# Kernel optimization log

Hardware: AMD Instinct MI355X
Metric: run time of the kernel (lower is better)

Reference implementation:

```python
import jax, jax.numpy as jnp
import numpy as np

B, S, D, H = 2, 2048, 1024, 16
DH = D // H  # 64


def setup_inputs() -> dict:
    key = jax.random.key(0)
    ks = jax.random.split(key, 9)
    def rn(k, shape, scale=1.0):
        return jax.random.normal(k, shape, dtype=jnp.float32) * scale
    w_scale = 1.0 / np.sqrt(D)
    return {
        "queries": rn(ks[0], (B, S, D)),
        "keys": rn(ks[1], (B, S, D)),
        "values": rn(ks[2], (B, S, D)),
        "Wq": rn(ks[3], (D, D), w_scale),
        "bq": rn(ks[4], (D,), w_scale),
        "Wk": rn(ks[5], (D, D), w_scale),
        "bk": rn(ks[6], (D,), w_scale),
        "Wv": rn(ks[7], (D, D), w_scale),
        "bv": rn(ks[8], (D,), w_scale),
    }


def _split_heads(x):
    # torch: cat(split(x, DH, dim=-1), dim=0) -> index (h*B + b); equivalent to
    # [B,S,H,DH] -> [H,B,S,DH]
    bsz, slen, _ = x.shape
    return x.reshape(bsz, slen, H, DH).transpose(2, 0, 1, 3)


def reference(queries, keys, values, Wq, bq, Wk, bk, Wv, bv):
    # Linear projections (W stored so that y = x @ W + b)
    Q = queries @ Wq + bq
    K = keys @ Wk + bk
    V = values @ Wv + bv

    Qh = _split_heads(Q)  # [H,B,S,DH]
    Kh = _split_heads(K)
    Vh = _split_heads(V)

    scale = 1.0 / jnp.sqrt(jnp.asarray(DH, dtype=Qh.dtype))
    scores = jnp.einsum("hbqd,hbkd->hbqk", Qh, Kh) * scale  # [H,B,S,S]
    attn = jax.nn.softmax(scores, axis=-1)  # dropout_rate=0 -> identity
    out = jnp.einsum("hbqk,hbkd->hbqd", attn, Vh)  # [H,B,S,DH]

    # torch: cat(split(out, B, dim=0), dim=2) -> [B,S,H*DH] with head h in slice h
    out = out.transpose(1, 2, 0, 3).reshape(queries.shape[0], queries.shape[1], D)
    return out + queries  # residual; NOTE: W_O is defined but unused in the original forward
```

## Files before the change

### kernel.cpp

```cpp
#include <hip/hip_runtime.h>
#include <hip/hip_bf16.h>
#include <math.h>

#define BB 2
#define SS 2048
#define DD 1024
#define HH 16
#define DHH 64
#define MM (BB * SS)

typedef float f32x4 __attribute__((ext_vector_type(4)));
typedef float f32x16 __attribute__((ext_vector_type(16)));
typedef __bf16 bf16x8 __attribute__((ext_vector_type(8)));
typedef unsigned int u32x2 __attribute__((ext_vector_type(2)));

#define N_QKV ((size_t)MM * DD)
#define N_W   ((size_t)DD * DD)

__device__ unsigned short g_X [3][N_QKV];
__device__ unsigned short g_Q [N_QKV];
__device__ unsigned short g_K [N_QKV];
__device__ unsigned short g_Vt[N_QKV];
__device__ unsigned short g_Wt[3][N_W];

__device__ __forceinline__ unsigned short f2bu(float f) {
    unsigned u = __float_as_uint(f);
    unsigned r = u + 0x7FFFu + ((u >> 16) & 1u);
    return (unsigned short)(r >> 16);
}

union FragU { uint4 u; bf16x8 v; unsigned short s[8]; };
static __device__ __forceinline__ bf16x8 ldfrag(const unsigned short* p) {
    FragU f; f.u = *(const uint4*)p; return f.v;
}

static __device__ __forceinline__ unsigned pkbf(float a, float b) {
    union { __bf16 h[2]; unsigned u; } w;
    w.h[0] = (__bf16)a; w.h[1] = (__bf16)b;
    return w.u;
}

static __device__ __forceinline__ float fexp2(float x) {
#if __has_builtin(__builtin_amdgcn_exp2f)
    return __builtin_amdgcn_exp2f(x);
#else
    float r;
    asm("v_exp_f32 %0, %1" : "=v"(r) : "v"(x));
    return r;
#endif
}

static __device__ __forceinline__ void plswap(unsigned &a, unsigned &b) {
#if __has_builtin(__builtin_amdgcn_permlane32_swap)
    u32x2 r = __builtin_amdgcn_permlane32_swap((int)a, (int)b, false, false);
    a = r[0]; b = r[1];
#else
    asm volatile("v_permlane32_swap_b32 %0, %1" : "+v"(a), "+v"(b));
#endif
}

__global__ __launch_bounds__(256) void cvt3(
        const float* __restrict__ x0, const float* __restrict__ x1,
        const float* __restrict__ x2, unsigned short* __restrict__ X)
{
    const float* src = blockIdx.y == 0 ? x0 : (blockIdx.y == 1 ? x1 : x2);
    unsigned short* dst = X + (size_t)blockIdx.y * N_QKV;
    const size_t i = ((size_t)blockIdx.x * 256 + threadIdx.x) * 4;
    const float4 v = *(const float4*)(src + i);
    ushort4 s;
    s.x = f2bu(v.x); s.y = f2bu(v.y); s.z = f2bu(v.z); s.w = f2bu(v.w);
    *(ushort4*)(dst + i) = s;
}

__global__ __launch_bounds__(256) void transpose_w3(
        const float* __restrict__ W0, const float* __restrict__ W1,
        const float* __restrict__ W2, unsigned short* __restrict__ Wt3)
{
    const float* W = blockIdx.z == 0 ? W0 : (blockIdx.z == 1 ? W1 : W2);
    unsigned short* Wt = Wt3 + (size_t)blockIdx.z * N_W;
    __shared__ float Ts[64][65];
    const int t = threadIdx.x;
    const int k0 = blockIdx.y * 64, n0 = blockIdx.x * 64;
#pragma unroll
    for (int i = 0; i < 16; ++i) {
        const int f = t + 256 * i, r = f >> 6, c = f & 63;
        Ts[r][c] = W[(size_t)(k0 + r) * DD + n0 + c];
    }
    __syncthreads();
#pragma unroll
    for (int i = 0; i < 16; ++i) {
        const int f = t + 256 * i, r = f >> 6, c = f & 63;
        Wt[(size_t)(n0 + r) * DD + k0 + c] = f2bu(Ts[c][r]);
    }
}

__global__ __launch_bounds__(256) void proj3(
        const unsigned short* __restrict__ X, const unsigned short* __restrict__ Wt3,
        const float* __restrict__ bq, const float* __restrict__ bk,
        const float* __restrict__ bv,
        unsigned short* __restrict__ Qp, unsigned short* __restrict__ Kp,
        unsigned short* __restrict__ Vtp)
{
    const int z = blockIdx.z;
    const unsigned short* xb = X   + (size_t)z * N_QKV;
    const unsigned short* Wt = Wt3 + (size_t)z * N_W;
    const float* bias = z == 0 ? bq : (z == 1 ? bk : bv);
    const float scale = z == 0 ? 0.18033688011112042f : 1.0f;

    __shared__ unsigned short As[128][72];
    __shared__ unsigned short Bs[128][72];
    const int t = threadIdx.x, lane = t & 63, w = t >> 6;
    const int q = lane >> 4, li = lane & 15;
    const int wm = (w >> 1) * 64, wn = (w & 1) * 64;
    const int m0 = blockIdx.y * 128, n0 = blockIdx.x * 128;
    const int rs = t >> 3, cs = (t & 7) * 8;

    f32x4 acc[4][4];
#pragma unroll
    for (int mt = 0; mt < 4; ++mt)
#pragma unroll
        for (int nt = 0; nt < 4; ++nt) acc[mt][nt] = (f32x4)0.f;

    uint4 pa0, pa1, pa2, pa3, pb0, pb1, pb2, pb3;
#define PROJ_LD(kk) \
    pa0 = *(const uint4*)(xb + (size_t)(m0 + rs      ) * DD + (kk) + cs); \
    pa1 = *(const uint4*)(xb + (size_t)(m0 + rs + 32 ) * DD + (kk) + cs); \
    pa2 = *(const uint4*)(xb + (size_t)(m0 + rs + 64 ) * DD + (kk) + cs); \
    pa3 = *(const uint4*)(xb + (size_t)(m0 + rs + 96 ) * DD + (kk) + cs); \
    pb0 = *(const uint4*)(Wt + (size_t)(n0 + rs      ) * DD + (kk) + cs); \
    pb1 = *(const uint4*)(Wt + (size_t)(n0 + rs + 32 ) * DD + (kk) + cs); \
    pb2 = *(const uint4*)(Wt + (size_t)(n0 + rs + 64 ) * DD + (kk) + cs); \
    pb3 = *(const uint4*)(Wt + (size_t)(n0 + rs + 96 ) * DD + (kk) + cs);

    PROJ_LD(0)

    for (int kk = 0; kk < DD; kk += 64) {
        *(uint4*)&As[rs     ][cs] = pa0;
        *(uint4*)&As[rs + 32][cs] = pa1;
        *(uint4*)&As[rs + 64][cs] = pa2;
        *(uint4*)&As[rs + 96][cs] = pa3;
        *(uint4*)&Bs[rs     ][cs] = pb0;
        *(uint4*)&Bs[rs + 32][cs] = pb1;
        *(uint4*)&Bs[rs + 64][cs] = pb2;
        *(uint4*)&Bs[rs + 96][cs] = pb3;
        __syncthreads();
        if (kk + 64 < DD) { PROJ_LD(kk + 64) }
#pragma unroll
        for (int ks = 0; ks < 64; ks += 32) {
            bf16x8 a[4], b[4];
#pragma unroll
            for (int mt = 0; mt < 4; ++mt) a[mt] = ldfrag(&As[wm + mt * 16 + li][ks + q * 8]);
#pragma unroll
            for (int nt = 0; nt < 4; ++nt) b[nt] = ldfrag(&Bs[wn + nt * 16 + li][ks + q * 8]);
#pragma unroll
            for (int mt = 0; mt < 4; ++mt)
#pragma unroll
                for (int nt = 0; nt < 4; ++nt)
                    acc[mt][nt] = __builtin_amdgcn_mfma_f32_16x16x32_bf16(
                        a[mt], b[nt], acc[mt][nt], 0, 0, 0);
        }
        __syncthreads();
    }
#undef PROJ_LD

    float bvv[4];
#pragma unroll
    for (int nt = 0; nt < 4; ++nt) bvv[nt] = bias[n0 + wn + nt * 16 + li];

    if (z < 2) {
        unsigned short* out = z == 0 ? Qp : Kp;
#pragma unroll
        for (int mt = 0; mt < 4; ++mt)
#pragma unroll
            for (int nt = 0; nt < 4; ++nt)
#pragma unroll
                for (int reg = 0; reg < 4; ++reg) {
                    const int m = m0 + wm + mt * 16 + q * 4 + reg;
                    out[(size_t)m * DD + n0 + wn + nt * 16 + li] =
                        f2bu((acc[mt][nt][reg] + bvv[nt]) * scale);
                }
    } else {
        const int b = m0 >> 11;
        const int h = (n0 + wn) >> 6;
#pragma unroll
        for (int mt = 0; mt < 4; ++mt)
#pragma unroll
            for (int nt = 0; nt < 4; ++nt) {
                const int s = (m0 & (SS - 1)) + wm + mt * 16 + q * 4;
                const int dh = nt * 16 + li;
                ushort4 sv;
                sv.x = f2bu(acc[mt][nt][0] + bvv[nt]);
                sv.y = f2bu(acc[mt][nt][1] + bvv[nt]);
                sv.z = f2bu(acc[mt][nt][2] + bvv[nt]);
                sv.w = f2bu(acc[mt][nt][3] + bvv[nt]);
                *(ushort4*)(Vtp + ((size_t)((b * HH + h) * DHH + dh)) * SS + s) = sv;
            }
    }
}

__global__ __launch_bounds__(512, 2) void attn8(
        const unsigned short* __restrict__ Qg, const unsigned short* __restrict__ Kg,
        const unsigned short* __restrict__ Vtg,
        const float* __restrict__ queries, float* __restrict__ outp)
{
    __shared__ unsigned short KVb[2][2][2][64][64];
    __shared__ float Lp[2][4][32];

    const int t = threadIdx.x, lane = t & 63;
    const int g  = t >> 8;
    const int wg = (t >> 6) & 3;
    const int col = lane & 31;
    const int hi  = lane >> 5;
    const int qt = blockIdx.x, h = blockIdx.y, b = blockIdx.z;

    const int tg = t & 255;
    const int sr = tg >> 3;
    const int sc = tg & 7;

    unsigned short (*Kb)[64][64] = KVb[g][0];
    unsigned short (*Vb)[64][64] = KVb[g][1];

    const unsigned short* Kbase = Kg  + (size_t)(b * SS) * DD + h * DHH;
    const unsigned short* Vbase = Vtg + ((size_t)((b * HH + h) * DHH)) * SS;

    bf16x8 qa[4];
    {
        const unsigned short* qp =
            Qg + (size_t)(b * SS + qt * 128 + wg * 32 + col) * DD + h * DHH + hi * 8;
#pragma unroll
        for (int i = 0; i < 4; ++i) qa[i] = ldfrag(qp + i * 16);
    }

    f32x16 o0 = (f32x16)0.f, o1 = (f32x16)0.f;
    float lsum = 0.f;
    const int xr2 = (col ^ (col >> 3)) & 7;
    const int wsw = (sr ^ (sr >> 3)) & 7;
    const int kvofs = g << 10;

    uint4 k0, k1, v0, v1;
#define LD_TILE(s0) \
    k0 = *(const uint4*)(Kbase + (size_t)((s0) + sr     ) * DD + sc * 8); \
    k1 = *(const uint4*)(Kbase + (size_t)((s0) + sr + 32) * DD + sc * 8); \
    v0 = *(const uint4*)(Vbase + (size_t)(sr     ) * SS + (s0) + sc * 8); \
    v1 = *(const uint4*)(Vbase + (size_t)(sr + 32) * SS + (s0) + sc * 8);

#define ST_TILE(buf) \
    *(uint4*)&Kb[buf][sr     ][(sc ^ wsw) * 8]     = k0; \
    *(uint4*)&Kb[buf][sr + 32][(sc ^ wsw ^ 4) * 8] = k1; \
    *(uint4*)&Vb[buf][sr     ][(sc ^ wsw) * 8]     = v0; \
    *(uint4*)&Vb[buf][sr + 32][(sc ^ wsw ^ 4) * 8] = v1;

    LD_TILE(kvofs)
    ST_TILE(0)
    __syncthreads();

    const int NT = 16;
#pragma unroll 2
    for (int kt = 0; kt < NT; ++kt) {
        const int cur = kt & 1;
        if (kt + 1 < NT) { LD_TILE(kvofs + (kt + 1) * 64) }

        f32x16 st0 = (f32x16)0.f, st1 = (f32x16)0.f;
#pragma unroll
        for (int i = 0; i < 4; ++i) {
            const int sl = (i * 2 + hi) ^ xr2;
            bf16x8 ka0 = ldfrag(&Kb[cur][col     ][sl * 8]);
            bf16x8 ka1 = ldfrag(&Kb[cur][col + 32][(sl ^ 4) * 8]);
            st0 = __builtin_amdgcn_mfma_f32_32x32x16_bf16(ka0, qa[i], st0, 0, 0, 0);
            st1 = __builtin_amdgcn_mfma_f32_32x32x16_bf16(ka1, qa[i], st1, 0, 0, 0);
        }

        unsigned pkw[4][4];
        float ls = 0.f;
#pragma unroll
        for (int s = 0; s < 2; ++s) {
            float pe[8];
#pragma unroll
            for (int r = 0; r < 8; ++r) pe[r] = fexp2(st0[8 * s + r]);
            ls += ((pe[0] + pe[1]) + (pe[2] + pe[3])) + ((pe[4] + pe[5]) + (pe[6] + pe[7]));
            pkw[s][0] = pkbf(pe[0], pe[1]); pkw[s][1] = pkbf(pe[2], pe[3]);
            pkw[s][2] = pkbf(pe[4], pe[5]); pkw[s][3] = pkbf(pe[6], pe[7]);
        }
#pragma unroll
        for (int s = 0; s < 2; ++s) {
            float pe[8];
#pragma unroll
            for (int r = 0; r < 8; ++r) pe[r] = fexp2(st1[8 * s + r]);
            ls += ((pe[0] + pe[1]) + (pe[2] + pe[3])) + ((pe[4] + pe[5]) + (pe[6] + pe[7]));
            pkw[2 + s][0] = pkbf(pe[0], pe[1]); pkw[2 + s][1] = pkbf(pe[2], pe[3]);
            pkw[2 + s][2] = pkbf(pe[4], pe[5]); pkw[2 + s][3] = pkbf(pe[6], pe[7]);
        }
        lsum += ls;

        if (kt + 1 < NT) { ST_TILE(cur ^ 1) }

#pragma unroll
        for (int c = 0; c < 4; ++c) {
            unsigned a0 = pkw[c][0], b0 = pkw[c][2];
            unsigned a1 = pkw[c][1], b1 = pkw[c][3];
            plswap(a0, b0);
            plswap(a1, b1);
            FragU pf;
            pf.u.x = a0; pf.u.y = a1; pf.u.z = b0; pf.u.w = b1;

            const int vl = (c * 2 + hi) ^ xr2;
            bf16x8 vb0 = ldfrag(&Vb[cur][col     ][vl * 8]);
            bf16x8 vb1 = ldfrag(&Vb[cur][col + 32][(vl ^ 4) * 8]);
            o0 = __builtin_amdgcn_mfma_f32_32x32x16_bf16(pf.v, vb0, o0, 0, 0, 0);
            o1 = __builtin_amdgcn_mfma_f32_32x32x16_bf16(pf.v, vb1, o1, 0, 0, 0);
        }
        __syncthreads();
    }
#undef LD_TILE
#undef ST_TILE

    const float lt = lsum + __shfl_xor(lsum, 32);
    float* Ob = (float*)KVb;
    const int obase = wg * 64 + lane;
    if (g == 1) {
#pragma unroll
        for (int r = 0; r < 16; ++r) {
            Ob[r * 256 + obase]        = o0[r];
            Ob[(16 + r) * 256 + obase] = o1[r];
        }
    }
    if (lane < 32) Lp[g][wg][lane] = lt;
    __syncthreads();

    if (g == 0) {
        const size_t gbase = (size_t)(b * SS + qt * 128 + wg * 32) * DD + h * DHH + col;
#pragma unroll
        for (int reg = 0; reg < 16; ++reg) {
            const int rl = (reg & 3) + 8 * (reg >> 2) + 4 * hi;
            const float li = 1.f / (Lp[0][wg][rl] + Lp[1][wg][rl]);
            const size_t gaddr = gbase + (size_t)rl * DD;
            outp[gaddr]      = (o0[reg] + Ob[reg * 256 + obase]) * li + queries[gaddr];
            outp[gaddr + 32] = (o1[reg] + Ob[(16 + reg) * 256 + obase]) * li + queries[gaddr + 32];
        }
    }
}

extern "C" void kernel_launch(void* const* d_in, const int* in_sizes, int n_in,
                              void* d_out, int out_size, void* d_ws, size_t ws_size,
                              hipStream_t stream) {
    const float* queries = (const float*)d_in[0];
    const float* keys    = (const float*)d_in[1];
    const float* values  = (const float*)d_in[2];
    const float* Wq      = (const float*)d_in[3];
    const float* bq      = (const float*)d_in[4];
    const float* Wk      = (const float*)d_in[5];
    const float* bk      = (const float*)d_in[6];
    const float* Wv      = (const float*)d_in[7];
    const float* bv      = (const float*)d_in[8];
    float* outp = (float*)d_out;

    const size_t need = (6 * N_QKV + 3 * N_W) * sizeof(unsigned short);
    unsigned short *Xp, *Qp, *Kp, *Vtp, *Wtp;
    if (ws_size >= need) {
        Xp  = (unsigned short*)d_ws;
        Qp  = Xp + 3 * N_QKV;
        Kp  = Qp + N_QKV;
        Vtp = Kp + N_QKV;
        Wtp = Vtp + N_QKV;
    } else {
        hipGetSymbolAddress((void**)&Xp,  HIP_SYMBOL(g_X));
        hipGetSymbolAddress((void**)&Qp,  HIP_SYMBOL(g_Q));
        hipGetSymbolAddress((void**)&Kp,  HIP_SYMBOL(g_K));
        hipGetSymbolAddress((void**)&Vtp, HIP_SYMBOL(g_Vt));
        hipGetSymbolAddress((void**)&Wtp, HIP_SYMBOL(g_Wt));
    }

    const dim3 bp(256);
    cvt3<<<dim3(MM * DD / 1024, 3), bp, 0, stream>>>(queries, keys, values, Xp);
    transpose_w3<<<dim3(16, 16, 3), bp, 0, stream>>>(Wq, Wk, Wv, Wtp);
    proj3<<<dim3(8, 32, 3), bp, 0, stream>>>(Xp, Wtp, bq, bk, bv, Qp, Kp, Vtp);
    attn8<<<dim3(SS / 128, HH, BB), dim3(512), 0, stream>>>(Qp, Kp, Vtp, queries, outp);
}
```

Before: 202.7 us.

## Deepen KV prefetch to two tiles, add MFMA priority, remap block order

The attention kernel now keeps two register sets of K/V tiles in flight, loading tile kt+2 while computing tile kt, so global load latency is hidden over a longer window. MFMA sections are wrapped in s_setprio to favour matrix issue over other waves. The grid is flattened to 1D and blocks are remapped so the eight consecutive block IDs cover different head/batch pairs, which changes L2 locality across XCDs. The extra prefetch registers raise register pressure under the 512x2 launch bound and may cause spills.

```diff
diff --git a/kernel.cpp b/kernel.cpp
--- a/kernel.cpp
+++ b/kernel.cpp
@@ -198,7 +198,7 @@
     }
 }
 
-__global__ __launch_bounds__(512, 2) void attn8(
+__global__ __launch_bounds__(512, 2) void attn9(
         const unsigned short* __restrict__ Qg, const unsigned short* __restrict__ Kg,
         const unsigned short* __restrict__ Vtg,
         const float* __restrict__ queries, float* __restrict__ outp)
@@ -211,7 +211,13 @@
     const int wg = (t >> 6) & 3;
     const int col = lane & 31;
     const int hi  = lane >> 5;
-    const int qt = blockIdx.x, h = blockIdx.y, b = blockIdx.z;
+
+    const int bid = blockIdx.x;
+    const int slot = bid >> 3;
+    const int p = (bid & 7) + 8 * (slot >> 4);
+    const int qt = slot & 15;
+    const int h = p & 15;
+    const int b = p >> 4;
 
     const int tg = t & 255;
     const int sr = tg >> 3;
@@ -237,82 +243,95 @@
     const int wsw = (sr ^ (sr >> 3)) & 7;
     const int kvofs = g << 10;
 
-    uint4 k0, k1, v0, v1;
-#define LD_TILE(s0) \
-    k0 = *(const uint4*)(Kbase + (size_t)((s0) + sr     ) * DD + sc * 8); \
-    k1 = *(const uint4*)(Kbase + (size_t)((s0) + sr + 32) * DD + sc * 8); \
-    v0 = *(const uint4*)(Vbase + (size_t)(sr     ) * SS + (s0) + sc * 8); \
-    v1 = *(const uint4*)(Vbase + (size_t)(sr + 32) * SS + (s0) + sc * 8);
-
-#define ST_TILE(buf) \
-    *(uint4*)&Kb[buf][sr     ][(sc ^ wsw) * 8]     = k0; \
-    *(uint4*)&Kb[buf][sr + 32][(sc ^ wsw ^ 4) * 8] = k1; \
-    *(uint4*)&Vb[buf][sr     ][(sc ^ wsw) * 8]     = v0; \
-    *(uint4*)&Vb[buf][sr + 32][(sc ^ wsw ^ 4) * 8] = v1;
-
-    LD_TILE(kvofs)
-    ST_TILE(0)
+    uint4 aK0, aK1, aV0, aV1, bK0, bK1, bV0, bV1;
+#define LD_SET(K0, K1, V0, V1, s0) \
+    K0 = *(const uint4*)(Kbase + (size_t)((s0) + sr     ) * DD + sc * 8); \
+    K1 = *(const uint4*)(Kbase + (size_t)((s0) + sr + 32) * DD + sc * 8); \
+    V0 = *(const uint4*)(Vbase + (size_t)(sr     ) * SS + (s0) + sc * 8); \
+    V1 = *(const uint4*)(Vbase + (size_t)(sr + 32) * SS + (s0) + sc * 8);
+
+#define ST_SET(K0, K1, V0, V1, buf) \
+    *(uint4*)&Kb[buf][sr     ][(sc ^ wsw) * 8]     = K0; \
+    *(uint4*)&Kb[buf][sr + 32][(sc ^ wsw ^ 4) * 8] = K1; \
+    *(uint4*)&Vb[buf][sr     ][(sc ^ wsw) * 8]     = V0; \
+    *(uint4*)&Vb[buf][sr + 32][(sc ^ wsw ^ 4) * 8] = V1;
+
+#define KT_BODY(CUR, LDG, STG, LDQ4, STQ4)                                    \
+    {                                                                         \
+        if (LDG) { LD_SET LDQ4 }                                              \
+                       \
+        f32x16 st0 = (f32x16)0.f, st1 = (f32x16)0.f;                          \
+        __builtin_amdgcn_s_setprio(1);                                        \
+        _Pragma("unroll")                                                     \
+        for (int i = 0; i < 4; ++i) {                                         \
+            const int sl = (i * 2 + hi) ^ xr2;                                \
+            bf16x8 ka0 = ldfrag(&Kb[CUR][col     ][sl * 8]);                  \
+            bf16x8 ka1 = ldfrag(&Kb[CUR][col + 32][(sl ^ 4) * 8]);            \
+            st0 = __builtin_amdgcn_mfma_f32_32x32x16_bf16(ka0, qa[i], st0, 0, 0, 0); \
+            st1 = __builtin_amdgcn_mfma_f32_32x32x16_bf16(ka1, qa[i], st1, 0, 0, 0); \
+        }                                                                     \
+        __builtin_amdgcn_s_setprio(0);                                        \
+                                 \
+        unsigned pkw[4][4];                                                   \
+        float ls = 0.f;                                                       \
+        _Pragma("unroll")                                                     \
+        for (int s = 0; s < 2; ++s) {                                         \
+            float pe[8];                                                      \
+            _Pragma("unroll")                                                 \
+            for (int r = 0; r < 8; ++r) pe[r] = fexp2(st0[8 * s + r]);        \
+            ls += ((pe[0] + pe[1]) + (pe[2] + pe[3])) + ((pe[4] + pe[5]) + (pe[6] + pe[7])); \
+            pkw[s][0] = pkbf(pe[0], pe[1]); pkw[s][1] = pkbf(pe[2], pe[3]);   \
+            pkw[s][2] = pkbf(pe[4], pe[5]); pkw[s][3] = pkbf(pe[6], pe[7]);   \
+        }                                                                     \
+        _Pragma("unroll")                                                     \
+        for (int s = 0; s < 2; ++s) {                                         \
+            float pe[8];                                                      \
+            _Pragma("unroll")                                                 \
+            for (int r = 0; r < 8; ++r) pe[r] = fexp2(st1[8 * s + r]);        \
+            ls += ((pe[0] + pe[1]) + (pe[2] + pe[3])) + ((pe[4] + pe[5]) + (pe[6] + pe[7])); \
+            pkw[2 + s][0] = pkbf(pe[0], pe[1]); pkw[2 + s][1] = pkbf(pe[2], pe[3]); \
+            pkw[2 + s][2] = pkbf(pe[4], pe[5]); pkw[2 + s][3] = pkbf(pe[6], pe[7]); \
+        }                                                                     \
+        lsum += ls;                                                           \
+             \
+        if (STG) { ST_SET STQ4 }                                              \
+          \
+        __builtin_amdgcn_s_setprio(1);                                        \
+        _Pragma("unroll")                                                     \
+        for (int c = 0; c < 4; ++c) {                                         \
+            unsigned A0 = pkw[c][0], B0 = pkw[c][2];                          \
+            unsigned A1 = pkw[c][1], B1 = pkw[c][3];                          \
+            plswap(A0, B0);                                                   \
+            plswap(A1, B1);                                                   \
+            FragU pf;                                                         \
+            pf.u.x = A0; pf.u.y = A1; pf.u.z = B0; pf.u.w = B1;               \
+            const int vl = (c * 2 + hi) ^ xr2;                                \
+            bf16x8 vb0 = ldfrag(&Vb[CUR][col     ][vl * 8]);                  \
+            bf16x8 vb1 = ldfrag(&Vb[CUR][col + 32][(vl ^ 4) * 8]);            \
+            o0 = __builtin_amdgcn_mfma_f32_32x32x16_bf16(pf.v, vb0, o0, 0, 0, 0); \
+            o1 = __builtin_amdgcn_mfma_f32_32x32x16_bf16(pf.v, vb1, o1, 0, 0, 0); \
+        }                                                                     \
+        __builtin_amdgcn_s_setprio(0);                                        \
+        __syncthreads();                                                      \
+    }
+
+    const int NT = 16;
+    LD_SET(aK0, aK1, aV0, aV1, kvofs)
+    LD_SET(bK0, bK1, bV0, bV1, kvofs + 64)
+    ST_SET(aK0, aK1, aV0, aV1, 0)
     __syncthreads();
 
-    const int NT = 16;
-#pragma unroll 2
-    for (int kt = 0; kt < NT; ++kt) {
-        const int cur = kt & 1;
-        if (kt + 1 < NT) { LD_TILE(kvofs + (kt + 1) * 64) }
-
-        f32x16 st0 = (f32x16)0.f, st1 = (f32x16)0.f;
-#pragma unroll
-        for (int i = 0; i < 4; ++i) {
-            const int sl = (i * 2 + hi) ^ xr2;
-            bf16x8 ka0 = ldfrag(&Kb[cur][col     ][sl * 8]);
-            bf16x8 ka1 = ldfrag(&Kb[cur][col + 32][(sl ^ 4) * 8]);
-            st0 = __builtin_amdgcn_mfma_f32_32x32x16_bf16(ka0, qa[i], st0, 0, 0, 0);
-            st1 = __builtin_amdgcn_mfma_f32_32x32x16_bf16(ka1, qa[i], st1, 0, 0, 0);
-        }
-
-        unsigned pkw[4][4];
-        float ls = 0.f;
-#pragma unroll
-        for (int s = 0; s < 2; ++s) {
-            float pe[8];
-#pragma unroll
-            for (int r = 0; r < 8; ++r) pe[r] = fexp2(st0[8 * s + r]);
-            ls += ((pe[0] + pe[1]) + (pe[2] + pe[3])) + ((pe[4] + pe[5]) + (pe[6] + pe[7]));
-            pkw[s][0] = pkbf(pe[0], pe[1]); pkw[s][1] = pkbf(pe[2], pe[3]);
-            pkw[s][2] = pkbf(pe[4], pe[5]); pkw[s][3] = pkbf(pe[6], pe[7]);
-        }
-#pragma unroll
-        for (int s = 0; s < 2; ++s) {
-            float pe[8];
-#pragma unroll
-            for (int r = 0; r < 8; ++r) pe[r] = fexp2(st1[8 * s + r]);
-            ls += ((pe[0] + pe[1]) + (pe[2] + pe[3])) + ((pe[4] + pe[5]) + (pe[6] + pe[7]));
-            pkw[2 + s][0] = pkbf(pe[0], pe[1]); pkw[2 + s][1] = pkbf(pe[2], pe[3]);
-            pkw[2 + s][2] = pkbf(pe[4], pe[5]); pkw[2 + s][3] = pkbf(pe[6], pe[7]);
-        }
-        lsum += ls;
-
-        if (kt + 1 < NT) { ST_TILE(cur ^ 1) }
-
-#pragma unroll
-        for (int c = 0; c < 4; ++c) {
-            unsigned a0 = pkw[c][0], b0 = pkw[c][2];
-            unsigned a1 = pkw[c][1], b1 = pkw[c][3];
-            plswap(a0, b0);
-            plswap(a1, b1);
-            FragU pf;
-            pf.u.x = a0; pf.u.y = a1; pf.u.z = b0; pf.u.w = b1;
-
-            const int vl = (c * 2 + hi) ^ xr2;
-            bf16x8 vb0 = ldfrag(&Vb[cur][col     ][vl * 8]);
-            bf16x8 vb1 = ldfrag(&Vb[cur][col + 32][(vl ^ 4) * 8]);
-            o0 = __builtin_amdgcn_mfma_f32_32x32x16_bf16(pf.v, vb0, o0, 0, 0, 0);
-            o1 = __builtin_amdgcn_mfma_f32_32x32x16_bf16(pf.v, vb1, o1, 0, 0, 0);
-        }
-        __syncthreads();
-    }
-#undef LD_TILE
-#undef ST_TILE
+    for (int kt = 0; kt < NT; kt += 2) {
+        KT_BODY(0, (kt + 2 < NT), (kt + 1 < NT),
+                (aK0, aK1, aV0, aV1, kvofs + (kt + 2) * 64),
+                (bK0, bK1, bV0, bV1, 1))
+        KT_BODY(1, (kt + 3 < NT), (kt + 2 < NT),
+                (bK0, bK1, bV0, bV1, kvofs + (kt + 3) * 64),
+                (aK0, aK1, aV0, aV1, 0))
+    }
+#undef KT_BODY
+#undef LD_SET
+#undef ST_SET
 
     const float lt = lsum + __shfl_xor(lsum, 32);
     float* Ob = (float*)KVb;
@@ -374,5 +393,5 @@
     cvt3<<<dim3(MM * DD / 1024, 3), bp, 0, stream>>>(queries, keys, values, Xp);
     transpose_w3<<<dim3(16, 16, 3), bp, 0, stream>>>(Wq, Wk, Wv, Wtp);
     proj3<<<dim3(8, 32, 3), bp, 0, stream>>>(Xp, Wtp, bq, bk, bv, Qp, Kp, Vtp);
-    attn8<<<dim3(SS / 128, HH, BB), dim3(512), 0, stream>>>(Qp, Kp, Vtp, queries, outp);
-}
+    attn9<<<dim3(512), dim3(512), 0, stream>>>(Qp, Kp, Vtp, queries, outp);
+}
```

Result: no change. 202.1 us (-0.3%).
